# Kernel optimization log

Hardware: AMD Instinct MI355X
Metric: run time of the kernel (lower is better)

The kernel has to match this reference:

```python
import jax, jax.numpy as jnp
import numpy as np

B, T, DIM = 2, 2048, 2048
N_HEADS, N_KV_HEADS = 16, 4
HEAD_DIM = DIM // N_HEADS  # 128
N_REP = N_HEADS // N_KV_HEADS  # 4
ROPE_THETA = 10000.0


def setup_inputs() -> dict:
    key = jax.random.key(0)
    ks = jax.random.split(key, 5)
    x = jax.random.normal(ks[0], (B, T, DIM), dtype=jnp.float32)
    # RoPE tables (equivalent to complex freqs_cis = exp(i * t * inv_freq))
    inv_freq = 1.0 / (ROPE_THETA ** (np.arange(0, HEAD_DIM, 2, dtype=np.float32) / HEAD_DIM))
    t = np.arange(T, dtype=np.float32)
    ang = np.outer(t, inv_freq)  # (T, HEAD_DIM//2)
    freqs_cos = jnp.asarray(np.cos(ang), dtype=jnp.float32)
    freqs_sin = jnp.asarray(np.sin(ang), dtype=jnp.float32)
    s = 0.02
    wq = jax.random.normal(ks[1], (DIM, N_HEADS * HEAD_DIM), dtype=jnp.float32) * s
    wk = jax.random.normal(ks[2], (DIM, N_KV_HEADS * HEAD_DIM), dtype=jnp.float32) * s
    wv = jax.random.normal(ks[3], (DIM, N_KV_HEADS * HEAD_DIM), dtype=jnp.float32) * s
    wo = jax.random.normal(ks[4], (N_HEADS * HEAD_DIM, DIM), dtype=jnp.float32) * s
    return {"x": x, "freqs_cos": freqs_cos, "freqs_sin": freqs_sin,
            "wq": wq, "wk": wk, "wv": wv, "wo": wo}


def _apply_rope(t, cos, sin):
    # t: (B, H, T, hd); cos/sin: (T, hd//2); interleaved pairs like view_as_complex
    tr = t[..., 0::2]
    ti = t[..., 1::2]
    c = cos[None, None, :, :]
    s = sin[None, None, :, :]
    out_r = tr * c - ti * s
    out_i = tr * s + ti * c
    return jnp.stack([out_r, out_i], axis=-1).reshape(t.shape)


def reference(x, freqs_cos, freqs_sin, wq, wk, wv, wo):
    Bb, Tt, C = x.shape
    q = (x @ wq).reshape(Bb, Tt, N_HEADS, HEAD_DIM).transpose(0, 2, 1, 3)      # (B,H,T,hd)
    k = (x @ wk).reshape(Bb, Tt, N_KV_HEADS, HEAD_DIM).transpose(0, 2, 1, 3)   # (B,KV,T,hd)
    v = (x @ wv).reshape(Bb, Tt, N_KV_HEADS, HEAD_DIM).transpose(0, 2, 1, 3)
    q = _apply_rope(q, freqs_cos[:Tt], freqs_sin[:Tt])
    k = _apply_rope(k, freqs_cos[:Tt], freqs_sin[:Tt])
    # GQA repeat_kv
    k = jnp.repeat(k, N_REP, axis=1)  # (B,H,T,hd)
    v = jnp.repeat(v, N_REP, axis=1)
    scale = 1.0 / jnp.sqrt(jnp.float32(HEAD_DIM))
    scores = jnp.einsum("bhqd,bhkd->bhqk", q, k) * scale
    causal = jnp.tril(jnp.ones((Tt, Tt), dtype=bool))
    scores = jnp.where(causal[None, None], scores, jnp.float32(-jnp.inf))
    attn = jax.nn.softmax(scores, axis=-1)
    out = jnp.einsum("bhqk,bhkd->bhqd", attn, v)          # (B,H,T,hd)
    out = out.transpose(0, 2, 1, 3).reshape(Bb, Tt, C)
    return out @ wo
```

## Files before the change

### kernel.cpp

```cpp
#include <hip/hip_runtime.h>
#include <hip/hip_bf16.h>

#define SEQT 2048
#define NH 16
#define HD 128

typedef __bf16 bf16;
typedef __bf16 bf16x4 __attribute__((ext_vector_type(4)));
typedef __bf16 bf16x8 __attribute__((ext_vector_type(8)));
typedef float f32x4 __attribute__((ext_vector_type(4)));
typedef float f32x16 __attribute__((ext_vector_type(16)));

__device__ inline void glds16(const bf16* g, bf16* l) {
  __builtin_amdgcn_global_load_lds(
      (const __attribute__((address_space(1))) unsigned int*)g,
      (__attribute__((address_space(3))) unsigned int*)l, 16, 0, 0);
}

__device__ inline unsigned int cvtpk(float a, float b) {
  unsigned int d;
  asm("v_cvt_pk_bf16_f32 %0, %1, %2" : "=v"(d) : "v"(a), "v"(b));
  return d;
}

__global__ __launch_bounds__(256) void k_convert(const float* __restrict__ in,
                                                 bf16* __restrict__ out, int n8) {
  int i = blockIdx.x * 256 + threadIdx.x;
  if (i >= n8) return;
  const float4* p = (const float4*)in + (size_t)i * 2;
  float4 a = p[0], b = p[1];
  bf16x8 o;
  o[0] = (bf16)a.x; o[1] = (bf16)a.y; o[2] = (bf16)a.z; o[3] = (bf16)a.w;
  o[4] = (bf16)b.x; o[5] = (bf16)b.y; o[6] = (bf16)b.z; o[7] = (bf16)b.w;
  *((bf16x8*)out + i) = o;
}

__global__ __launch_bounds__(256) void k_transpose(const float* __restrict__ in,
                                                   bf16* __restrict__ out, int R, int C) {
  __shared__ float tile[32][33];
  int c0 = blockIdx.x * 32, r0 = blockIdx.y * 32;
  int tx = threadIdx.x, ty = threadIdx.y;
#pragma unroll
  for (int i = 0; i < 4; i++)
    tile[ty + i * 8][tx] = in[(size_t)(r0 + ty + i * 8) * C + c0 + tx];
  __syncthreads();
#pragma unroll
  for (int i = 0; i < 4; i++) {
    int r = ty + i * 8;
    out[(size_t)(c0 + r) * R + r0 + tx] = (bf16)tile[tx][r];
  }
}

template <typename OutT>
__global__ __launch_bounds__(256) void k_gemm(const bf16* __restrict__ A,
                                              const bf16* __restrict__ Bt,
                                              OutT* __restrict__ C,
                                              int M, int N, int K, int ldc) {
  __shared__ bf16 Al[128 * 32];
  __shared__ bf16 Bl[128 * 32];
  int tid = threadIdx.x;
  int m0 = blockIdx.y * 128, n0 = blockIdx.x * 128;
  int wid = tid >> 6, lane = tid & 63;
  int wr = (wid >> 1) * 64, wc = (wid & 1) * 64;
  int lr = lane & 15, lk = (lane >> 4) * 8;
  f32x4 acc[4][4] = {};

  for (int k0 = 0; k0 < K; k0 += 32) {
#pragma unroll
    for (int i = 0; i < 2; i++) {
      int idx = i * 256 + tid;
      int r = idx >> 2, kc = (idx & 3) * 8;
      glds16(A + (size_t)(m0 + r) * K + k0 + kc, Al + idx * 8);
      glds16(Bt + (size_t)(n0 + r) * K + k0 + kc, Bl + idx * 8);
    }
    __syncthreads();
    bf16x8 af[4], bfr[4];
#pragma unroll
    for (int mi = 0; mi < 4; mi++) af[mi] = *(const bf16x8*)&Al[(wr + mi * 16 + lr) * 32 + lk];
#pragma unroll
    for (int ni = 0; ni < 4; ni++) bfr[ni] = *(const bf16x8*)&Bl[(wc + ni * 16 + lr) * 32 + lk];
#pragma unroll
    for (int mi = 0; mi < 4; mi++)
#pragma unroll
      for (int ni = 0; ni < 4; ni++)
        acc[mi][ni] = __builtin_amdgcn_mfma_f32_16x16x32_bf16(af[mi], bfr[ni], acc[mi][ni], 0, 0, 0);
    __syncthreads();
  }

  int rbase = m0 + wr + ((lane >> 4) << 2);
#pragma unroll
  for (int mi = 0; mi < 4; mi++)
#pragma unroll
    for (int ni = 0; ni < 4; ni++)
#pragma unroll
      for (int r = 0; r < 4; r++) {
        int row = rbase + mi * 16 + r;
        int col = n0 + wc + ni * 16 + lr;
        C[(size_t)row * ldc + col] = (OutT)acc[mi][ni][r];
      }
}

__global__ __launch_bounds__(256) void k_rope(bf16* __restrict__ qkv,
                                              const float* __restrict__ fcos,
                                              const float* __restrict__ fsin) {
  int gid = blockIdx.x * 256 + threadIdx.x;
  int row = gid / 1280;
  int p = gid % 1280;
  int head = p >> 6;
  int dp = p & 63;
  int t = row & (SEQT - 1);
  int colbase = head < NH ? head * HD : NH * HD + (head - NH) * HD;
  bf16* ptr = qkv + (size_t)row * 3072 + colbase + dp * 2;
  float a = (float)ptr[0], b = (float)ptr[1];
  float c = fcos[t * 64 + dp], s = fsin[t * 64 + dp];
  ptr[0] = (bf16)(a * c - b * s);
  ptr[1] = (bf16)(a * s + b * c);
}

__global__ __launch_bounds__(256, 2) void k_attn(const bf16* __restrict__ qkv,
                                                 bf16* __restrict__ attout) {
  __shared__ bf16 Kl[2][64 * 128];
  __shared__ bf16 Vt[128][72];
  __shared__ float Atab[4][32];
  int bid = blockIdx.x;
  int qt = 15 - (bid >> 5);
  int bh = bid & 31;
  int b = bh >> 4, h = bh & 15, kvh = h >> 2;
  int tid = threadIdx.x, wid = tid >> 6, lane = tid & 63;
  int li = lane & 31, hi = lane >> 5;
  int q0 = qt * 128;
  int qmin = q0 + wid * 32, qmax = qmin + 31;
  int qlane = qmin + li;
  const float C1 = 0.12751744979927212f;

  const bf16* kgbase = qkv + (size_t)b * SEQT * 3072 + 2048 + kvh * HD;
  const bf16* vgbase = kgbase + 512;

  bf16x8 qf[8];
  {
    const bf16* qb = qkv + (size_t)(b * SEQT + qlane) * 3072 + h * HD + hi * 8;
#pragma unroll
    for (int ks = 0; ks < 8; ks++) qf[ks] = *(const bf16x8*)(qb + ks * 16);
  }

  float mrun = -INFINITY, lpart = 0.f;
  f32x16 o0 = {}, o1 = {}, o2 = {}, o3 = {};
  int nkt = 2 * qt + 2;

  int g = (lane >> 4) & 3;
  int lr = lane & 15;
  int kq4 = (wid * 4 + g) * 4;
  int dc = lr * 8;
  int xr = (lr & 7) << 3;
  int kvw = kq4 ^ xr;

  bf16x8 vr0, vr1, vr2, vr3;

#pragma unroll
  for (int r = 0; r < 4; r++) {
    int ci = r * 256 + tid;
    int row = ci >> 4;
    int sl = (ci & 15) ^ (row & 15);
    glds16(kgbase + (size_t)row * 3072 + sl * 8, &Kl[0][ci * 8]);
  }
  {
    const bf16* vrow = vgbase + (size_t)kq4 * 3072 + dc;
    vr0 = *(const bf16x8*)(vrow);
    vr1 = *(const bf16x8*)(vrow + 3072);
    vr2 = *(const bf16x8*)(vrow + 6144);
    vr3 = *(const bf16x8*)(vrow + 9216);
  }

  for (int kt = 0; kt < nkt; kt++) {
    int cur = kt & 1;
    int kv0 = kt * 64;
    asm volatile("s_waitcnt vmcnt(0)" ::: "memory");

#pragma unroll
    for (int j = 0; j < 8; j++) {
      bf16x4 w;
      w[0] = vr0[j]; w[1] = vr1[j]; w[2] = vr2[j]; w[3] = vr3[j];
      *(bf16x4*)&Vt[dc + j][kvw] = w;
    }

    if (kt + 1 < nkt) {
      int kv1 = kv0 + 64;
      bf16* kdst = &Kl[cur ^ 1][0];
#pragma unroll
      for (int r = 0; r < 4; r++) {
        int ci = r * 256 + tid;
        int row = ci >> 4;
        int sl = (ci & 15) ^ (row & 15);
        glds16(kgbase + (size_t)(kv1 + row) * 3072 + sl * 8, kdst + ci * 8);
      }
      const bf16* vrow = vgbase + (size_t)(kv1 + kq4) * 3072 + dc;
      vr0 = *(const bf16x8*)(vrow);
      vr1 = *(const bf16x8*)(vrow + 3072);
      vr2 = *(const bf16x8*)(vrow + 6144);
      vr3 = *(const bf16x8*)(vrow + 9216);
    }

    asm volatile("s_waitcnt lgkmcnt(0)" ::: "memory");
    __builtin_amdgcn_sched_barrier(0);
    __builtin_amdgcn_s_barrier();
    __builtin_amdgcn_sched_barrier(0);

    if (kv0 <= qmax) {
      f32x16 s0 = {}, s1 = {};
      const char* kb0 = (const char*)&Kl[cur][0] + li * 256;
      __builtin_amdgcn_s_setprio(1);
#pragma unroll
      for (int ks = 0; ks < 8; ks++) {
        int off = ((ks * 2 + hi) ^ (li & 15)) << 4;
        bf16x8 kf0 = *(const bf16x8*)(kb0 + off);
        bf16x8 kf1 = *(const bf16x8*)(kb0 + 8192 + off);
        s0 = __builtin_amdgcn_mfma_f32_32x32x16_bf16(kf0, qf[ks], s0, 0, 0, 0);
        s1 = __builtin_amdgcn_mfma_f32_32x32x16_bf16(kf1, qf[ks], s1, 0, 0, 0);
      }
      __builtin_amdgcn_s_setprio(0);

      if (kv0 + 63 > qmin) {
        int base0 = kv0 + 4 * hi - qlane;
#pragma unroll
        for (int r = 0; r < 16; r++) {
          int off = (r & 3) + 8 * (r >> 2);
          if (base0 + off > 0) s0[r] = -INFINITY;
          if (base0 + 32 + off > 0) s1[r] = -INFINITY;
        }
      }

      float pm = s0[0];
#pragma unroll
      for (int r = 1; r < 16; r++) pm = fmaxf(pm, s0[r]);
#pragma unroll
      for (int r = 0; r < 16; r++) pm = fmaxf(pm, s1[r]);
      pm = fmaxf(pm, __shfl_xor(pm, 32));

      if (!__all(pm - mrun <= 62.0f)) {
        float mnew = fmaxf(mrun, pm);
        float alpha = exp2f((mrun - mnew) * C1);
        mrun = mnew;
        lpart *= alpha;
        Atab[wid][li] = alpha;
        asm volatile("s_waitcnt lgkmcnt(0)" ::: "memory");
        f32x4 a0 = *(const f32x4*)&Atab[wid][4 * hi];
        f32x4 a1 = *(const f32x4*)&Atab[wid][4 * hi + 8];
        f32x4 a2 = *(const f32x4*)&Atab[wid][4 * hi + 16];
        f32x4 a3 = *(const f32x4*)&Atab[wid][4 * hi + 24];
#define RESC_RR(rr, av)                                            \
  _Pragma("unroll") for (int i = 0; i < 4; i++) {                  \
    float f = av[i];                                               \
    o0[rr * 4 + i] *= f; o1[rr * 4 + i] *= f;                      \
    o2[rr * 4 + i] *= f; o3[rr * 4 + i] *= f;                      \
  }
        RESC_RR(0, a0) RESC_RR(1, a1) RESC_RR(2, a2) RESC_RR(3, a3)
#undef RESC_RR
      }

      float mC = mrun * C1;
      float rs = 0.f;
#pragma unroll
      for (int r = 0; r < 16; r++) {
        float p = exp2f(fmaf(s0[r], C1, -mC));
        s0[r] = p; rs += p;
      }
#pragma unroll
      for (int r = 0; r < 16; r++) {
        float p = exp2f(fmaf(s1[r], C1, -mC));
        s1[r] = p; rs += p;
      }
      lpart += rs;

      union U4 { unsigned int u[4]; bf16x8 v; };
      U4 pa0, pa1, pa2, pa3;
      {
        unsigned int e0 = cvtpk(s0[0], s0[1]), e1 = cvtpk(s0[2], s0[3]);
        unsigned int e2 = cvtpk(s0[4], s0[5]), e3 = cvtpk(s0[6], s0[7]);
        unsigned int e4 = cvtpk(s0[8], s0[9]), e5 = cvtpk(s0[10], s0[11]);
        unsigned int e6 = cvtpk(s0[12], s0[13]), e7 = cvtpk(s0[14], s0[15]);
        unsigned int t0 = __shfl_xor(e0, 32), t1 = __shfl_xor(e1, 32);
        unsigned int t2 = __shfl_xor(e2, 32), t3 = __shfl_xor(e3, 32);
        unsigned int t4 = __shfl_xor(e4, 32), t5 = __shfl_xor(e5, 32);
        unsigned int t6 = __shfl_xor(e6, 32), t7 = __shfl_xor(e7, 32);
        pa0.u[0] = hi ? t2 : e0;  pa0.u[1] = hi ? t3 : e1;
        pa0.u[2] = hi ? e2 : t0;  pa0.u[3] = hi ? e3 : t1;
        pa1.u[0] = hi ? t6 : e4;  pa1.u[1] = hi ? t7 : e5;
        pa1.u[2] = hi ? e6 : t4;  pa1.u[3] = hi ? e7 : t5;
        unsigned int f0 = cvtpk(s1[0], s1[1]), f1 = cvtpk(s1[2], s1[3]);
        unsigned int f2 = cvtpk(s1[4], s1[5]), f3 = cvtpk(s1[6], s1[7]);
        unsigned int f4 = cvtpk(s1[8], s1[9]), f5 = cvtpk(s1[10], s1[11]);
        unsigned int f6 = cvtpk(s1[12], s1[13]), f7 = cvtpk(s1[14], s1[15]);
        unsigned int u0 = __shfl_xor(f0, 32), u1 = __shfl_xor(f1, 32);
        unsigned int u2 = __shfl_xor(f2, 32), u3 = __shfl_xor(f3, 32);
        unsigned int u4 = __shfl_xor(f4, 32), u5 = __shfl_xor(f5, 32);
        unsigned int u6 = __shfl_xor(f6, 32), u7 = __shfl_xor(f7, 32);
        pa2.u[0] = hi ? u2 : f0;  pa2.u[1] = hi ? u3 : f1;
        pa2.u[2] = hi ? f2 : u0;  pa2.u[3] = hi ? f3 : u1;
        pa3.u[0] = hi ? u6 : f4;  pa3.u[1] = hi ? u7 : f5;
        pa3.u[2] = hi ? f6 : u4;  pa3.u[3] = hi ? f7 : u5;
      }

      __builtin_amdgcn_s_setprio(1);
#define PV_DB(OACC, DB)                                                      \
  {                                                                          \
    int d = DB * 32 + li;                                                    \
    int xv = ((d >> 3) & 7) << 3;                                            \
    bf16x8 vb0 = *(const bf16x8*)&Vt[d][(hi * 8) ^ xv];                      \
    bf16x8 vb1 = *(const bf16x8*)&Vt[d][(16 + hi * 8) ^ xv];                 \
    bf16x8 vb2 = *(const bf16x8*)&Vt[d][(32 + hi * 8) ^ xv];                 \
    bf16x8 vb3 = *(const bf16x8*)&Vt[d][(48 + hi * 8) ^ xv];                 \
    OACC = __builtin_amdgcn_mfma_f32_32x32x16_bf16(pa0.v, vb0, OACC, 0, 0, 0); \
    OACC = __builtin_amdgcn_mfma_f32_32x32x16_bf16(pa1.v, vb1, OACC, 0, 0, 0); \
    OACC = __builtin_amdgcn_mfma_f32_32x32x16_bf16(pa2.v, vb2, OACC, 0, 0, 0); \
    OACC = __builtin_amdgcn_mfma_f32_32x32x16_bf16(pa3.v, vb3, OACC, 0, 0, 0); \
  }
      PV_DB(o0, 0) PV_DB(o1, 1) PV_DB(o2, 2) PV_DB(o3, 3)
#undef PV_DB
      __builtin_amdgcn_s_setprio(0);
    }

    __builtin_amdgcn_sched_barrier(0);
    __builtin_amdgcn_s_barrier();
    __builtin_amdgcn_sched_barrier(0);
  }

  lpart += __shfl_xor(lpart, 32);
  Atab[wid][li] = 1.f / lpart;
  asm volatile("s_waitcnt lgkmcnt(0)" ::: "memory");
  f32x4 l0 = *(const f32x4*)&Atab[wid][4 * hi];
  f32x4 l1 = *(const f32x4*)&Atab[wid][4 * hi + 8];
  f32x4 l2 = *(const f32x4*)&Atab[wid][4 * hi + 16];
  f32x4 l3 = *(const f32x4*)&Atab[wid][4 * hi + 24];
  {
    size_t obase = (size_t)(b * SEQT) * 2048 + h * HD;
#define STORE_RR(rr, lv)                                                     \
  _Pragma("unroll") for (int i = 0; i < 4; i++) {                            \
    int q = qmin + 4 * hi + 8 * rr + i;                                      \
    size_t rowb = obase + (size_t)q * 2048 + li;                             \
    attout[rowb + 0]  = (bf16)(o0[rr * 4 + i] * lv[i]);                      \
    attout[rowb + 32] = (bf16)(o1[rr * 4 + i] * lv[i]);                      \
    attout[rowb + 64] = (bf16)(o2[rr * 4 + i] * lv[i]);                      \
    attout[rowb + 96] = (bf16)(o3[rr * 4 + i] * lv[i]);                      \
  }
    STORE_RR(0, l0) STORE_RR(1, l1) STORE_RR(2, l2) STORE_RR(3, l3)
#undef STORE_RR
  }
}

extern "C" void kernel_launch(void* const* d_in, const int* in_sizes, int n_in,
                              void* d_out, int out_size, void* d_ws, size_t ws_size,
                              hipStream_t stream) {
  const float* x    = (const float*)d_in[0];
  const float* fcos = (const float*)d_in[1];
  const float* fsin = (const float*)d_in[2];
  const float* wq   = (const float*)d_in[3];
  const float* wk   = (const float*)d_in[4];
  const float* wv   = (const float*)d_in[5];
  const float* wo   = (const float*)d_in[6];
  float* out = (float*)d_out;

  char* ws = (char*)d_ws;
  bf16* XB  = (bf16*)ws;
  bf16* W   = (bf16*)(ws + 16777216);
  bf16* QKV = (bf16*)(ws + 16777216 + 12582912);

  dim3 tb(32, 8);
  k_transpose<<<dim3(64, 64), tb, 0, stream>>>(wq, W, 2048, 2048);
  k_transpose<<<dim3(16, 64), tb, 0, stream>>>(wk, W + 2048 * 2048, 2048, 512);
  k_transpose<<<dim3(16, 64), tb, 0, stream>>>(wv, W + 2560 * 2048, 2048, 512);
  k_convert<<<4096, 256, 0, stream>>>(x, XB, 1048576);
  k_gemm<bf16><<<dim3(24, 32), 256, 0, stream>>>(XB, W, QKV, 4096, 3072, 2048, 3072);
  k_rope<<<20480, 256, 0, stream>>>(QKV, fcos, fsin);
  k_attn<<<512, 256, 0, stream>>>(QKV, XB);
  k_transpose<<<dim3(64, 64), tb, 0, stream>>>(wo, W, 2048, 2048);
  k_gemm<float><<<dim3(16, 32), 256, 0, stream>>>(XB, W, out, 4096, 2048, 2048, 2048);
}
```

Before: 241.6 us.

## Split KV tiles across two wave groups per attention block and merge

The attention block grows from 4 to 8 waves. Two wave groups take alternating KV tiles for the same 128 query rows, each keeping its own online-softmax state. V now sits in a double-buffered LDS tile, and the next-tile loads are issued after the per-iteration barrier, which removes the second barrier. At the end the groups merge their max, sum and partial outputs through LDS, reusing the K buffer. The aim is more waves per CU to hide latency and half the serial KV loop per wave, in exchange for more LDS per block and an extra reduction step.

```diff
diff --git a/kernel.cpp b/kernel.cpp
--- a/kernel.cpp
+++ b/kernel.cpp
@@ -6,6 +6,7 @@
 #define HD 128
 
 typedef __bf16 bf16;
+typedef __bf16 bf16x2 __attribute__((ext_vector_type(2)));
 typedef __bf16 bf16x4 __attribute__((ext_vector_type(4)));
 typedef __bf16 bf16x8 __attribute__((ext_vector_type(8)));
 typedef float f32x4 __attribute__((ext_vector_type(4)));
@@ -117,19 +118,20 @@
   ptr[1] = (bf16)(a * s + b * c);
 }
 
-__global__ __launch_bounds__(256, 2) void k_attn(const bf16* __restrict__ qkv,
+__global__ __launch_bounds__(512, 4) void k_attn(const bf16* __restrict__ qkv,
                                                  bf16* __restrict__ attout) {
-  __shared__ bf16 Kl[2][64 * 128];
-  __shared__ bf16 Vt[128][72];
-  __shared__ float Atab[4][32];
+  __shared__ bf16 Kl[2][8192];
+  __shared__ bf16 Vt[2][128][72];
+  __shared__ float Tabs[4][8][32];
   int bid = blockIdx.x;
   int qt = 15 - (bid >> 5);
   int bh = bid & 31;
   int b = bh >> 4, h = bh & 15, kvh = h >> 2;
   int tid = threadIdx.x, wid = tid >> 6, lane = tid & 63;
+  int grp = wid >> 2, wq = wid & 3;
   int li = lane & 31, hi = lane >> 5;
   int q0 = qt * 128;
-  int qmin = q0 + wid * 32, qmax = qmin + 31;
+  int qmin = q0 + wq * 32, qmax = qmin + 31;
   int qlane = qmin + li;
   const float C1 = 0.12751744979927212f;
 
@@ -147,28 +149,25 @@
   f32x16 o0 = {}, o1 = {}, o2 = {}, o3 = {};
   int nkt = 2 * qt + 2;
 
-  int g = (lane >> 4) & 3;
-  int lr = lane & 15;
-  int kq4 = (wid * 4 + g) * 4;
-  int dc = lr * 8;
-  int xr = (lr & 7) << 3;
-  int kvw = kq4 ^ xr;
-
-  bf16x8 vr0, vr1, vr2, vr3;
-
-#pragma unroll
-  for (int r = 0; r < 4; r++) {
-    int ci = r * 256 + tid;
+  int rp = tid >> 4;
+  int lv = tid & 15;
+  int dcv = lv * 8;
+  int xrv = (lv & 7) << 3;
+  int kvwv = (2 * rp) ^ xrv;
+
+  bf16x8 vrA, vrB;
+
+#pragma unroll
+  for (int r = 0; r < 2; r++) {
+    int ci = r * 512 + tid;
     int row = ci >> 4;
     int sl = (ci & 15) ^ (row & 15);
     glds16(kgbase + (size_t)row * 3072 + sl * 8, &Kl[0][ci * 8]);
   }
   {
-    const bf16* vrow = vgbase + (size_t)kq4 * 3072 + dc;
-    vr0 = *(const bf16x8*)(vrow);
-    vr1 = *(const bf16x8*)(vrow + 3072);
-    vr2 = *(const bf16x8*)(vrow + 6144);
-    vr3 = *(const bf16x8*)(vrow + 9216);
+    const bf16* vrow = vgbase + (size_t)(2 * rp) * 3072 + dcv;
+    vrA = *(const bf16x8*)(vrow);
+    vrB = *(const bf16x8*)(vrow + 3072);
   }
 
   for (int kt = 0; kt < nkt; kt++) {
@@ -178,26 +177,9 @@
 
 #pragma unroll
     for (int j = 0; j < 8; j++) {
-      bf16x4 w;
-      w[0] = vr0[j]; w[1] = vr1[j]; w[2] = vr2[j]; w[3] = vr3[j];
-      *(bf16x4*)&Vt[dc + j][kvw] = w;
-    }
-
-    if (kt + 1 < nkt) {
-      int kv1 = kv0 + 64;
-      bf16* kdst = &Kl[cur ^ 1][0];
-#pragma unroll
-      for (int r = 0; r < 4; r++) {
-        int ci = r * 256 + tid;
-        int row = ci >> 4;
-        int sl = (ci & 15) ^ (row & 15);
-        glds16(kgbase + (size_t)(kv1 + row) * 3072 + sl * 8, kdst + ci * 8);
-      }
-      const bf16* vrow = vgbase + (size_t)(kv1 + kq4) * 3072 + dc;
-      vr0 = *(const bf16x8*)(vrow);
-      vr1 = *(const bf16x8*)(vrow + 3072);
-      vr2 = *(const bf16x8*)(vrow + 6144);
-      vr3 = *(const bf16x8*)(vrow + 9216);
+      bf16x2 w;
+      w[0] = vrA[j]; w[1] = vrB[j];
+      *(bf16x2*)&Vt[cur][dcv + j][kvwv] = w;
     }
 
     asm volatile("s_waitcnt lgkmcnt(0)" ::: "memory");
@@ -205,7 +187,22 @@
     __builtin_amdgcn_s_barrier();
     __builtin_amdgcn_sched_barrier(0);
 
-    if (kv0 <= qmax) {
+    if (kt + 1 < nkt) {
+      int kv1 = kv0 + 64;
+      bf16* kdst = &Kl[cur ^ 1][0];
+#pragma unroll
+      for (int r = 0; r < 2; r++) {
+        int ci = r * 512 + tid;
+        int row = ci >> 4;
+        int sl = (ci & 15) ^ (row & 15);
+        glds16(kgbase + (size_t)(kv1 + row) * 3072 + sl * 8, kdst + ci * 8);
+      }
+      const bf16* vrow = vgbase + (size_t)(kv1 + 2 * rp) * 3072 + dcv;
+      vrA = *(const bf16x8*)(vrow);
+      vrB = *(const bf16x8*)(vrow + 3072);
+    }
+
+    if (grp == cur && kv0 <= qmax) {
       f32x16 s0 = {}, s1 = {};
       const char* kb0 = (const char*)&Kl[cur][0] + li * 256;
       __builtin_amdgcn_s_setprio(1);
@@ -241,12 +238,12 @@
         float alpha = exp2f((mrun - mnew) * C1);
         mrun = mnew;
         lpart *= alpha;
-        Atab[wid][li] = alpha;
+        Tabs[0][wid][li] = alpha;
         asm volatile("s_waitcnt lgkmcnt(0)" ::: "memory");
-        f32x4 a0 = *(const f32x4*)&Atab[wid][4 * hi];
-        f32x4 a1 = *(const f32x4*)&Atab[wid][4 * hi + 8];
-        f32x4 a2 = *(const f32x4*)&Atab[wid][4 * hi + 16];
-        f32x4 a3 = *(const f32x4*)&Atab[wid][4 * hi + 24];
+        f32x4 a0 = *(const f32x4*)&Tabs[0][wid][4 * hi];
+        f32x4 a1 = *(const f32x4*)&Tabs[0][wid][4 * hi + 8];
+        f32x4 a2 = *(const f32x4*)&Tabs[0][wid][4 * hi + 16];
+        f32x4 a3 = *(const f32x4*)&Tabs[0][wid][4 * hi + 24];
 #define RESC_RR(rr, av)                                            \
   _Pragma("unroll") for (int i = 0; i < 4; i++) {                  \
     float f = av[i];                                               \
@@ -305,10 +302,10 @@
   {                                                                          \
     int d = DB * 32 + li;                                                    \
     int xv = ((d >> 3) & 7) << 3;                                            \
-    bf16x8 vb0 = *(const bf16x8*)&Vt[d][(hi * 8) ^ xv];                      \
-    bf16x8 vb1 = *(const bf16x8*)&Vt[d][(16 + hi * 8) ^ xv];                 \
-    bf16x8 vb2 = *(const bf16x8*)&Vt[d][(32 + hi * 8) ^ xv];                 \
-    bf16x8 vb3 = *(const bf16x8*)&Vt[d][(48 + hi * 8) ^ xv];                 \
+    bf16x8 vb0 = *(const bf16x8*)&Vt[cur][d][(hi * 8) ^ xv];                 \
+    bf16x8 vb1 = *(const bf16x8*)&Vt[cur][d][(16 + hi * 8) ^ xv];            \
+    bf16x8 vb2 = *(const bf16x8*)&Vt[cur][d][(32 + hi * 8) ^ xv];            \
+    bf16x8 vb3 = *(const bf16x8*)&Vt[cur][d][(48 + hi * 8) ^ xv];            \
     OACC = __builtin_amdgcn_mfma_f32_32x32x16_bf16(pa0.v, vb0, OACC, 0, 0, 0); \
     OACC = __builtin_amdgcn_mfma_f32_32x32x16_bf16(pa1.v, vb1, OACC, 0, 0, 0); \
     OACC = __builtin_amdgcn_mfma_f32_32x32x16_bf16(pa2.v, vb2, OACC, 0, 0, 0); \
@@ -318,20 +315,63 @@
 #undef PV_DB
       __builtin_amdgcn_s_setprio(0);
     }
-
-    __builtin_amdgcn_sched_barrier(0);
+  }
+
+  lpart += __shfl_xor(lpart, 32);
+  Tabs[0][wid][li] = mrun;
+  Tabs[1][wid][li] = lpart;
+  asm volatile("s_waitcnt lgkmcnt(0)" ::: "memory");
+  __builtin_amdgcn_s_barrier();
+  int peer = wid ^ 4;
+  float mP = Tabs[0][peer][li], lP = Tabs[1][peer][li];
+  float mS = fmaxf(mrun, mP);
+  float fMe = exp2f((mrun - mS) * C1);
+  float fPe = exp2f((mP - mS) * C1);
+  float lTot = lpart * fMe + lP * fPe;
+  Tabs[2][wid][li] = fMe;
+  Tabs[3][wid][li] = 1.f / lTot;
+  asm volatile("s_waitcnt lgkmcnt(0)" ::: "memory");
+  __builtin_amdgcn_s_barrier();
+  f32x4 Fv0 = *(const f32x4*)&Tabs[2][wid][4 * hi];
+  f32x4 Fv1 = *(const f32x4*)&Tabs[2][wid][4 * hi + 8];
+  f32x4 Fv2 = *(const f32x4*)&Tabs[2][wid][4 * hi + 16];
+  f32x4 Fv3 = *(const f32x4*)&Tabs[2][wid][4 * hi + 24];
+  f32x4 Iv0 = *(const f32x4*)&Tabs[3][wid][4 * hi];
+  f32x4 Iv1 = *(const f32x4*)&Tabs[3][wid][4 * hi + 8];
+  f32x4 Iv2 = *(const f32x4*)&Tabs[3][wid][4 * hi + 16];
+  f32x4 Iv3 = *(const f32x4*)&Tabs[3][wid][4 * hi + 24];
+
+  float* X = (float*)&Kl[0][0];
+  float* Xb = X + (wid & 1) * 4096;
+#pragma unroll
+  for (int round = 0; round < 2; round++) {
+    if (((wid & 2) >> 1) == round && grp == 1) {
+#define XW_RR(OACC, DB, rr, Fv)                                              \
+  _Pragma("unroll") for (int i = 0; i < 4; i++)                              \
+    Xb[(4 * hi + 8 * rr + i) * 128 + DB * 32 + li] = OACC[rr * 4 + i] * Fv[i];
+#define XW_DB(OACC, DB) XW_RR(OACC, DB, 0, Fv0) XW_RR(OACC, DB, 1, Fv1) \
+                        XW_RR(OACC, DB, 2, Fv2) XW_RR(OACC, DB, 3, Fv3)
+      XW_DB(o0, 0) XW_DB(o1, 1) XW_DB(o2, 2) XW_DB(o3, 3)
+#undef XW_DB
+#undef XW_RR
+    }
+    asm volatile("s_waitcnt lgkmcnt(0)" ::: "memory");
     __builtin_amdgcn_s_barrier();
-    __builtin_amdgcn_sched_barrier(0);
-  }
-
-  lpart += __shfl_xor(lpart, 32);
-  Atab[wid][li] = 1.f / lpart;
-  asm volatile("s_waitcnt lgkmcnt(0)" ::: "memory");
-  f32x4 l0 = *(const f32x4*)&Atab[wid][4 * hi];
-  f32x4 l1 = *(const f32x4*)&Atab[wid][4 * hi + 8];
-  f32x4 l2 = *(const f32x4*)&Atab[wid][4 * hi + 16];
-  f32x4 l3 = *(const f32x4*)&Atab[wid][4 * hi + 24];
-  {
+    if (((wid & 2) >> 1) == round && grp == 0) {
+#define XR_RR(OACC, DB, rr, Fv)                                              \
+  _Pragma("unroll") for (int i = 0; i < 4; i++)                              \
+    OACC[rr * 4 + i] = OACC[rr * 4 + i] * Fv[i] +                            \
+        Xb[(4 * hi + 8 * rr + i) * 128 + DB * 32 + li];
+#define XR_DB(OACC, DB) XR_RR(OACC, DB, 0, Fv0) XR_RR(OACC, DB, 1, Fv1) \
+                        XR_RR(OACC, DB, 2, Fv2) XR_RR(OACC, DB, 3, Fv3)
+      XR_DB(o0, 0) XR_DB(o1, 1) XR_DB(o2, 2) XR_DB(o3, 3)
+#undef XR_DB
+#undef XR_RR
+    }
+    __builtin_amdgcn_s_barrier();
+  }
+
+  if (grp == 0) {
     size_t obase = (size_t)(b * SEQT) * 2048 + h * HD;
 #define STORE_RR(rr, lv)                                                     \
   _Pragma("unroll") for (int i = 0; i < 4; i++) {                            \
@@ -342,7 +382,7 @@
     attout[rowb + 64] = (bf16)(o2[rr * 4 + i] * lv[i]);                      \
     attout[rowb + 96] = (bf16)(o3[rr * 4 + i] * lv[i]);                      \
   }
-    STORE_RR(0, l0) STORE_RR(1, l1) STORE_RR(2, l2) STORE_RR(3, l3)
+    STORE_RR(0, Iv0) STORE_RR(1, Iv1) STORE_RR(2, Iv2) STORE_RR(3, Iv3)
 #undef STORE_RR
   }
 }
@@ -371,7 +411,7 @@
   k_convert<<<4096, 256, 0, stream>>>(x, XB, 1048576);
   k_gemm<bf16><<<dim3(24, 32), 256, 0, stream>>>(XB, W, QKV, 4096, 3072, 2048, 3072);
   k_rope<<<20480, 256, 0, stream>>>(QKV, fcos, fsin);
-  k_attn<<<512, 256, 0, stream>>>(QKV, XB);
+  k_attn<<<512, 512, 0, stream>>>(QKV, XB);
   k_transpose<<<dim3(64, 64), tb, 0, stream>>>(wo, W, 2048, 2048);
   k_gemm<float><<<dim3(16, 32), 256, 0, stream>>>(XB, W, out, 4096, 2048, 2048, 2048);
 }
```

Result: slower. 482.8 us (+99.9%).
